# Optimization experiments

Measured on AMD Instinct MI355X. Metric: run time of the kernel, lower is better.

Reference implementation:

```python
import jax, jax.numpy as jnp
import numpy as np

D = 1024
H = 16
DEPTH = D // H


def setup_inputs() -> dict:
    key = jax.random.key(0)
    ks = jax.random.split(key, 10)
    B, S = 4, 2048
    scale = 1.0 / np.sqrt(D)
    x = jax.random.normal(ks[0], (B, S, D), dtype=jnp.float32)
    attention_mask = jnp.ones((B, S, S), dtype=jnp.int32)
    Wq = jax.random.normal(ks[1], (D, D), dtype=jnp.float32) * scale
    bq = jnp.zeros((D,), dtype=jnp.float32)
    Wk = jax.random.normal(ks[2], (D, D), dtype=jnp.float32) * scale
    bk = jnp.zeros((D,), dtype=jnp.float32)
    Wv = jax.random.normal(ks[3], (D, D), dtype=jnp.float32) * scale
    bv = jnp.zeros((D,), dtype=jnp.float32)
    Wo = jax.random.normal(ks[4], (D, D), dtype=jnp.float32) * scale
    bo = jnp.zeros((D,), dtype=jnp.float32)
    return {"x": x, "attention_mask": attention_mask,
            "Wq": Wq, "bq": bq, "Wk": Wk, "bk": bk,
            "Wv": Wv, "bv": bv, "Wo": Wo, "bo": bo}


def _split_heads(t):
    # [b, s, h*d] -> [b, h, s, d]
    b, s, _ = t.shape
    return t.reshape(b, s, H, DEPTH).transpose(0, 2, 1, 3)


def reference(x, attention_mask, Wq, bq, Wk, bk, Wv, bv, Wo, bo):
    # QKV projections (torch Linear: x @ W.T + b; here W stored as [in, out])
    q = _split_heads(x @ Wq + bq)  # [b, h, s, d]
    k = _split_heads(x @ Wk + bk)
    v = _split_heads(x @ Wv + bv)
    scores = jnp.einsum('bhsd,bhtd->bhst', q, k) / jnp.sqrt(jnp.float32(DEPTH))
    mask = attention_mask[:, None, :, :]  # [b, 1, s, s]
    scores = jnp.where(mask == 0, jnp.float32(-jnp.inf), scores)
    attn = jax.nn.softmax(scores, axis=-1)
    # Dropout is identity in eval mode
    out = jnp.einsum('bhst,bhtd->bhsd', attn, v)  # [b, h, s, d]
    b, h, s, d = out.shape
    out = out.transpose(0, 2, 1, 3).reshape(b, s, h * d)
    return out @ Wo + bo
```

## Files before the change

kernel.cpp:

```cpp
#include <hip/hip_runtime.h>
#include <hip/hip_bf16.h>

typedef __bf16 bf16;
typedef __bf16 bf16x4 __attribute__((ext_vector_type(4)));
typedef __bf16 bf16x8 __attribute__((ext_vector_type(8)));
typedef float f32x4 __attribute__((ext_vector_type(4)));

#define AS1 __attribute__((address_space(1)))
#define AS3 __attribute__((address_space(3)))

__device__ __forceinline__ void gload_lds16(const void* g, void* l) {
  __builtin_amdgcn_global_load_lds((const AS1 void*)g, (AS3 void*)l, 16, 0, 0);
}

__device__ __forceinline__ float fexp2(float x) {
#if __has_builtin(__builtin_amdgcn_exp2f)
  return __builtin_amdgcn_exp2f(x);
#else
  return exp2f(x);
#endif
}

#define BB 4
#define SS 2048
#define DD 1024
#define HH 16
#define MM (BB*SS)
#define LDQ 3072
#define NT (SS/64)
#define QSCALE 0.18033688011112042f

__global__ __launch_bounds__(256) void cvt_x(const float* __restrict__ x,
                                             bf16* __restrict__ xb) {
  int i = (blockIdx.x * 256 + threadIdx.x) * 8;
  float4 a = *(const float4*)&x[i];
  float4 b = *(const float4*)&x[i + 4];
  bf16x8 o;
  o[0] = (bf16)a.x; o[1] = (bf16)a.y; o[2] = (bf16)a.z; o[3] = (bf16)a.w;
  o[4] = (bf16)b.x; o[5] = (bf16)b.y; o[6] = (bf16)b.z; o[7] = (bf16)b.w;
  *(bf16x8*)&xb[i] = o;
}

__global__ __launch_bounds__(256) void wtrans4(const float* __restrict__ W0,
                                               const float* __restrict__ W1,
                                               const float* __restrict__ W2,
                                               const float* __restrict__ W3,
                                               bf16* __restrict__ WtQKV,
                                               bf16* __restrict__ Wto) {
  __shared__ float t[64][65];
  const int which = blockIdx.z;
  const float* W = which == 0 ? W0 : which == 1 ? W1 : which == 2 ? W2 : W3;
  bf16* Wt = which < 3 ? WtQKV + (size_t)which * 1024 * DD : Wto;
  const float scale = (which == 0) ? QSCALE : 1.0f;
  int bi = blockIdx.y, bj = blockIdx.x;
  for (int c = 0; c < 16; c++) {
    int idx = threadIdx.x + c * 256;
    int r = idx >> 6, col = idx & 63;
    t[r][col] = W[(size_t)(bi * 64 + r) * DD + bj * 64 + col];
  }
  __syncthreads();
  for (int c = 0; c < 16; c++) {
    int idx = threadIdx.x + c * 256;
    int rn = idx >> 6, ck = idx & 63;
    Wt[(size_t)(bj * 64 + rn) * DD + bi * 64 + ck] = (bf16)(t[ck][rn] * scale);
  }
}

__global__ void bias_cat(const float* __restrict__ bq, const float* __restrict__ bk,
                         const float* __restrict__ bv, float* __restrict__ ball,
                         int* __restrict__ flag) {
  int i = blockIdx.x * 256 + threadIdx.x;
  if (i == 0) *flag = 1;
  float v = (i < 1024) ? bq[i] * QSCALE
                       : ((i < 2048) ? bk[i - 1024] : bv[i - 2048]);
  ball[i] = v;
}

__global__ __launch_bounds__(256) void mask_check(const int4* __restrict__ m,
                                                  int n4, int* flag) {
  int ok = 1;
  for (int i = blockIdx.x * 256 + threadIdx.x; i < n4; i += gridDim.x * 256) {
    int4 v = m[i];
    if (!(v.x && v.y && v.z && v.w)) ok = 0;
  }
  if (__ballot(!ok)) {
    if ((threadIdx.x & 63) == 0) atomicAnd(flag, 0);
  }
}

__global__ __launch_bounds__(256) void vtrans(const bf16* __restrict__ QKV,
                                              bf16* __restrict__ Vt) {
  __shared__ bf16 t[64][80];
  int b = blockIdx.x >> 5, st = blockIdx.x & 31, nt = blockIdx.y;
  int tid = threadIdx.x;
  #pragma unroll
  for (int c = 0; c < 2; c++) {
    int idx = tid + c * 256;
    int r = idx >> 3;
    int c8 = (idx & 7) * 8;
    *(bf16x8*)&t[r][c8] =
        *(const bf16x8*)&QKV[(size_t)(b * SS + st * 64 + r) * LDQ + 2048 +
                             nt * 64 + c8];
  }
  __syncthreads();
  #pragma unroll
  for (int c = 0; c < 2; c++) {
    int idx = tid + c * 256;
    int rn = idx >> 3;
    int s8 = (idx & 7) * 8;
    bf16x8 v;
    #pragma unroll
    for (int j = 0; j < 8; j++) v[j] = t[s8 + j][rn];
    *(bf16x8*)&Vt[(size_t)(b * 1024 + nt * 64 + rn) * SS + st * 64 + s8] = v;
  }
}

template <int OUT_BF16>
__global__ __launch_bounds__(256) void gemm_bt(const bf16* __restrict__ A,
                                               const bf16* __restrict__ Bt,
                                               const float* __restrict__ bias,
                                               void* __restrict__ Cout, int ldc) {
  constexpr int K = 1024;
  constexpr int BM = 128, BN = 128, BK = 64;
  __shared__ bf16 As[BM * BK];
  __shared__ bf16 Bs[BN * BK];
  const int tid = threadIdx.x;
  const int w = tid >> 6, l = tid & 63;
  const int wm = w >> 1, wn = w & 1;
  const int by = blockIdx.x, bx = blockIdx.y;

  f32x4 acc[4][4] = {};

  const int sRow = l >> 3;
  const int sSlot = (l & 7) ^ sRow;
  const bf16* aBase = A + (size_t)(by * BM + w * 32 + sRow) * K + sSlot * 8;
  const bf16* bBase = Bt + (size_t)(bx * BN + w * 32 + sRow) * K + sSlot * 8;

  for (int k0 = 0; k0 < K; k0 += BK) {
    #pragma unroll
    for (int c = 0; c < 4; c++) {
      gload_lds16(aBase + (size_t)(c * 8) * K + k0, &As[(w * 32 + c * 8) * BK]);
      gload_lds16(bBase + (size_t)(c * 8) * K + k0, &Bs[(w * 32 + c * 8) * BK]);
    }
    __syncthreads();
    #pragma unroll
    for (int kk = 0; kk < 2; kk++) {
      bf16x8 af[4], bfr[4];
      #pragma unroll
      for (int i = 0; i < 4; i++) {
        int row = wm * 64 + i * 16 + (l & 15);
        int sl = (kk * 4 + (l >> 4)) ^ (row & 7);
        af[i] = *(const bf16x8*)(&As[row * BK + sl * 8]);
      }
      #pragma unroll
      for (int j = 0; j < 4; j++) {
        int row = wn * 64 + j * 16 + (l & 15);
        int sl = (kk * 4 + (l >> 4)) ^ (row & 7);
        bfr[j] = *(const bf16x8*)(&Bs[row * BK + sl * 8]);
      }
      #pragma unroll
      for (int i = 0; i < 4; i++)
        #pragma unroll
        for (int j = 0; j < 4; j++)
          acc[i][j] = __builtin_amdgcn_mfma_f32_16x16x32_bf16(af[i], bfr[j],
                                                              acc[i][j], 0, 0, 0);
    }
    __syncthreads();
  }

  #pragma unroll
  for (int j = 0; j < 4; j++) {
    int col = bx * BN + wn * 64 + j * 16 + (l & 15);
    float bb = bias[col];
    #pragma unroll
    for (int i = 0; i < 4; i++) {
      int row0 = by * BM + wm * 64 + i * 16 + (l >> 4) * 4;
      #pragma unroll
      for (int r = 0; r < 4; r++) {
        float v = acc[i][j][r] + bb;
        if (OUT_BF16)
          ((bf16*)Cout)[(size_t)(row0 + r) * ldc + col] = (bf16)v;
        else
          ((float*)Cout)[(size_t)(row0 + r) * ldc + col] = v;
      }
    }
  }
}

__global__ __launch_bounds__(256, 2) void attn_fwd(const bf16* __restrict__ QKV,
                                                   const bf16* __restrict__ Vt,
                                                   const int* __restrict__ mask,
                                                   const int* __restrict__ flag,
                                                   bf16* __restrict__ att) {
  __shared__ bf16 Ks[2][64 * 64];
  __shared__ bf16 Vs[2][64 * 64];
  const int tid = threadIdx.x, w = tid >> 6, l = tid & 63;
  const int g = l >> 4, q = l & 15;
  const int bh = blockIdx.x, b = bh >> 4, h = bh & 15;
  const int q0 = blockIdx.y * 256 + w * 64;
  const bool allones = (*flag != 0);

  bf16x8 bq[4][2];
  #pragma unroll
  for (int qb = 0; qb < 4; qb++) {
    const bf16* qptr =
        QKV + (size_t)(b * SS + q0 + qb * 16 + q) * LDQ + h * 64 + g * 8;
    bq[qb][0] = *(const bf16x8*)qptr;
    bq[qb][1] = *(const bf16x8*)(qptr + 32);
  }

  bf16x8 ones;
  #pragma unroll
  for (int j = 0; j < 8; j++) ones[j] = (bf16)1.0f;

  f32x4 o[4][4] = {};
  f32x4 ls[4] = {};

  const int sSlot = (l & 7) ^ ((l >> 3) & 7);
  const bf16* kPtr[2];
  #pragma unroll
  for (int c = 0; c < 2; c++) {
    int B8 = 2 * w + c;
    int tl = 32 * (B8 >> 2) + 16 * (B8 & 1) + 4 * ((B8 >> 1) & 1) +
             8 * (l >> 5) + ((l >> 3) & 3);
    kPtr[c] = QKV + (size_t)(b * SS + tl) * LDQ + 1024 + h * 64 + sSlot * 8;
  }
  const bf16* vBase =
      Vt + (size_t)(b * 1024 + h * 64 + w * 16 + (l >> 3)) * SS + sSlot * 8;

  gload_lds16(kPtr[0], &Ks[0][(2 * w + 0) * 8 * 64]);
  gload_lds16(kPtr[1], &Ks[0][(2 * w + 1) * 8 * 64]);
  gload_lds16(vBase, &Vs[0][(w * 16) * 64]);
  gload_lds16(vBase + (size_t)8 * SS, &Vs[0][(w * 16 + 8) * 64]);

  for (int it = 0; it < NT; ++it) {
    const int cur = it & 1;
    if (it + 1 < NT) {
      const int t1 = (it + 1) * 64;
      gload_lds16(kPtr[0] + (size_t)t1 * LDQ, &Ks[cur ^ 1][(2 * w + 0) * 8 * 64]);
      gload_lds16(kPtr[1] + (size_t)t1 * LDQ, &Ks[cur ^ 1][(2 * w + 1) * 8 * 64]);
      gload_lds16(vBase + t1, &Vs[cur ^ 1][(w * 16) * 64]);
      gload_lds16(vBase + (size_t)8 * SS + t1, &Vs[cur ^ 1][(w * 16 + 8) * 64]);
      asm volatile("s_waitcnt vmcnt(4)" ::: "memory");
    } else {
      asm volatile("s_waitcnt vmcnt(0)" ::: "memory");
    }
    __builtin_amdgcn_s_barrier();
    asm volatile("" ::: "memory");

    const bf16* ks = Ks[cur];
    const bf16* vs = Vs[cur];

    bf16x8 af[4][2];
    #pragma unroll
    for (int tt = 0; tt < 4; tt++) {
      int row = tt * 16 + q;
      af[tt][0] = *(const bf16x8*)(&ks[row * 64 + (g ^ (q & 7)) * 8]);
      af[tt][1] = *(const bf16x8*)(&ks[row * 64 + (((4 + g) ^ (q & 7))) * 8]);
    }

    bf16x8 pb[4][2];
    #pragma unroll
    for (int qb = 0; qb < 4; qb++) {
      f32x4 s4[4];
      #pragma unroll
      for (int tt = 0; tt < 4; tt++) {
        f32x4 z = {};
        z = __builtin_amdgcn_mfma_f32_16x16x32_bf16(af[tt][0], bq[qb][0], z, 0, 0, 0);
        z = __builtin_amdgcn_mfma_f32_16x16x32_bf16(af[tt][1], bq[qb][1], z, 0, 0, 0);
        s4[tt] = z;
      }

      if (!allones) {
        const int t0 = it * 64;
        #pragma unroll
        for (int tt = 0; tt < 4; tt++)
          #pragma unroll
          for (int r = 0; r < 4; r++) {
            int tl = 32 * (tt >> 1) + 8 * g + 4 * (tt & 1) + r;
            if (mask[(size_t)(b * SS + q0 + qb * 16 + q) * SS + t0 + tl] == 0)
              s4[tt][r] = -1e30f;
          }
      }

      #pragma unroll
      for (int kk = 0; kk < 2; kk++) {
        bf16x8 f;
        #pragma unroll
        for (int j = 0; j < 8; j++)
          f[j] = (bf16)fexp2(s4[2 * kk + (j >> 2)][j & 3]);
        pb[qb][kk] = f;
      }
      ls[qb] = __builtin_amdgcn_mfma_f32_16x16x32_bf16(ones, pb[qb][0], ls[qb], 0, 0, 0);
      ls[qb] = __builtin_amdgcn_mfma_f32_16x16x32_bf16(ones, pb[qb][1], ls[qb], 0, 0, 0);
    }

    __builtin_amdgcn_s_setprio(1);
    #pragma unroll
    for (int kk = 0; kk < 2; kk++) {
      int cc = kk * 4 + g;
      #pragma unroll
      for (int n = 0; n < 4; n++) {
        int vrow = n * 16 + q;
        int vsl = cc ^ (q & 7);
        bf16x8 av = *(const bf16x8*)(&vs[vrow * 64 + vsl * 8]);
        #pragma unroll
        for (int qb = 0; qb < 4; qb++)
          o[qb][n] = __builtin_amdgcn_mfma_f32_16x16x32_bf16(av, pb[qb][kk],
                                                             o[qb][n], 0, 0, 0);
      }
    }
    __builtin_amdgcn_s_setprio(0);

    asm volatile("" ::: "memory");
    __builtin_amdgcn_s_barrier();
    asm volatile("" ::: "memory");
  }

  #pragma unroll
  for (int qb = 0; qb < 4; qb++) {
    float inv = 1.0f / ls[qb][0];
    #pragma unroll
    for (int n = 0; n < 4; n++) {
      bf16x4 ov;
      #pragma unroll
      for (int r = 0; r < 4; r++) ov[r] = (bf16)(o[qb][n][r] * inv);
      *(bf16x4*)&att[(size_t)(b * SS + q0 + qb * 16 + q) * DD + h * 64 +
                     n * 16 + g * 4] = ov;
    }
  }
}

extern "C" void kernel_launch(void* const* d_in, const int* in_sizes, int n_in,
                              void* d_out, int out_size, void* d_ws, size_t ws_size,
                              hipStream_t stream) {
  const float* x = (const float*)d_in[0];
  const int* mask = (const int*)d_in[1];
  const float* Wq = (const float*)d_in[2];
  const float* bq = (const float*)d_in[3];
  const float* Wk = (const float*)d_in[4];
  const float* bk = (const float*)d_in[5];
  const float* Wv = (const float*)d_in[6];
  const float* bv = (const float*)d_in[7];
  const float* Wo = (const float*)d_in[8];
  const float* bo = (const float*)d_in[9];
  float* out = (float*)d_out;

  char* p = (char*)d_ws;
  const size_t MB16 = (size_t)MM * DD * 2;
  bf16* xb = (bf16*)p;   p += MB16;
  bf16* QKV = (bf16*)p;  p += (size_t)MM * LDQ * 2;
  bf16* Vt = (bf16*)p;   p += MB16;
  bf16* Wt_all = (bf16*)p; p += (size_t)3072 * DD * 2;
  bf16* Wot = (bf16*)p;  p += (size_t)DD * DD * 2;
  float* ball = (float*)p; p += 3072 * 4;
  int* flag = (int*)p;
  bf16* att = xb;

  bias_cat<<<12, 256, 0, stream>>>(bq, bk, bv, ball, flag);
  mask_check<<<1024, 256, 0, stream>>>((const int4*)mask, BB * SS * SS / 4, flag);
  cvt_x<<<MM * DD / (256 * 8), 256, 0, stream>>>(x, xb);
  wtrans4<<<dim3(16, 16, 4), 256, 0, stream>>>(Wq, Wk, Wv, Wo, Wt_all, Wot);

  gemm_bt<1><<<dim3(64, 24), 256, 0, stream>>>(xb, Wt_all, ball, QKV, LDQ);
  vtrans<<<dim3(128, 16), 256, 0, stream>>>(QKV, Vt);
  attn_fwd<<<dim3(BB * HH, SS / 256), 256, 0, stream>>>(QKV, Vt, mask, flag, att);
  gemm_bt<0><<<dim3(64, 8), 256, 0, stream>>>(att, Wot, bo, out, DD);
}
```

Before: 188.8 us.

## Fuse prep kernels, write V transposed from QKV GEMM, fold mask check into GEMM

Merges the x conversion, weight transposes and bias concatenation into one launch. The QKV GEMM epilogue now writes the V part straight into the transposed Vt buffer, which removes the separate vtrans kernel. The mask all-ones scan moves into the tail of the QKV GEMM. Together these cut kernel launches and a full V round trip through memory. In exchange the GEMM does extra mask reads after its main loop, and the flag init and mask scan now live in different kernels, which relies on stream ordering.

Result: faster. 179.4 us (-5.0%).

```diff
diff --git a/kernel.cpp b/kernel.cpp
--- a/kernel.cpp
+++ b/kernel.cpp
@@ -30,96 +30,59 @@
 #define NT (SS/64)
 #define QSCALE 0.18033688011112042f
 
-__global__ __launch_bounds__(256) void cvt_x(const float* __restrict__ x,
-                                             bf16* __restrict__ xb) {
-  int i = (blockIdx.x * 256 + threadIdx.x) * 8;
-  float4 a = *(const float4*)&x[i];
-  float4 b = *(const float4*)&x[i + 4];
-  bf16x8 o;
-  o[0] = (bf16)a.x; o[1] = (bf16)a.y; o[2] = (bf16)a.z; o[3] = (bf16)a.w;
-  o[4] = (bf16)b.x; o[5] = (bf16)b.y; o[6] = (bf16)b.z; o[7] = (bf16)b.w;
-  *(bf16x8*)&xb[i] = o;
-}
-
-__global__ __launch_bounds__(256) void wtrans4(const float* __restrict__ W0,
-                                               const float* __restrict__ W1,
-                                               const float* __restrict__ W2,
-                                               const float* __restrict__ W3,
-                                               bf16* __restrict__ WtQKV,
-                                               bf16* __restrict__ Wto) {
+__global__ __launch_bounds__(256) void prep(
+    const float* __restrict__ x, bf16* __restrict__ xb,
+    const float* __restrict__ Wq, const float* __restrict__ Wk,
+    const float* __restrict__ Wv, const float* __restrict__ Wo,
+    bf16* __restrict__ WtQKV, bf16* __restrict__ Wto,
+    const float* __restrict__ bq, const float* __restrict__ bk,
+    const float* __restrict__ bv, float* __restrict__ ball,
+    int* __restrict__ flag) {
   __shared__ float t[64][65];
-  const int which = blockIdx.z;
-  const float* W = which == 0 ? W0 : which == 1 ? W1 : which == 2 ? W2 : W3;
-  bf16* Wt = which < 3 ? WtQKV + (size_t)which * 1024 * DD : Wto;
-  const float scale = (which == 0) ? QSCALE : 1.0f;
-  int bi = blockIdx.y, bj = blockIdx.x;
-  for (int c = 0; c < 16; c++) {
-    int idx = threadIdx.x + c * 256;
-    int r = idx >> 6, col = idx & 63;
-    t[r][col] = W[(size_t)(bi * 64 + r) * DD + bj * 64 + col];
-  }
-  __syncthreads();
-  for (int c = 0; c < 16; c++) {
-    int idx = threadIdx.x + c * 256;
-    int rn = idx >> 6, ck = idx & 63;
-    Wt[(size_t)(bj * 64 + rn) * DD + bi * 64 + ck] = (bf16)(t[ck][rn] * scale);
-  }
-}
-
-__global__ void bias_cat(const float* __restrict__ bq, const float* __restrict__ bk,
-                         const float* __restrict__ bv, float* __restrict__ ball,
-                         int* __restrict__ flag) {
-  int i = blockIdx.x * 256 + threadIdx.x;
-  if (i == 0) *flag = 1;
-  float v = (i < 1024) ? bq[i] * QSCALE
-                       : ((i < 2048) ? bk[i - 1024] : bv[i - 2048]);
-  ball[i] = v;
-}
-
-__global__ __launch_bounds__(256) void mask_check(const int4* __restrict__ m,
-                                                  int n4, int* flag) {
-  int ok = 1;
-  for (int i = blockIdx.x * 256 + threadIdx.x; i < n4; i += gridDim.x * 256) {
-    int4 v = m[i];
-    if (!(v.x && v.y && v.z && v.w)) ok = 0;
-  }
-  if (__ballot(!ok)) {
-    if ((threadIdx.x & 63) == 0) atomicAnd(flag, 0);
-  }
-}
-
-__global__ __launch_bounds__(256) void vtrans(const bf16* __restrict__ QKV,
-                                              bf16* __restrict__ Vt) {
-  __shared__ bf16 t[64][80];
-  int b = blockIdx.x >> 5, st = blockIdx.x & 31, nt = blockIdx.y;
-  int tid = threadIdx.x;
-  #pragma unroll
-  for (int c = 0; c < 2; c++) {
-    int idx = tid + c * 256;
-    int r = idx >> 3;
-    int c8 = (idx & 7) * 8;
-    *(bf16x8*)&t[r][c8] =
-        *(const bf16x8*)&QKV[(size_t)(b * SS + st * 64 + r) * LDQ + 2048 +
-                             nt * 64 + c8];
-  }
-  __syncthreads();
-  #pragma unroll
-  for (int c = 0; c < 2; c++) {
-    int idx = tid + c * 256;
-    int rn = idx >> 3;
-    int s8 = (idx & 7) * 8;
-    bf16x8 v;
-    #pragma unroll
-    for (int j = 0; j < 8; j++) v[j] = t[s8 + j][rn];
-    *(bf16x8*)&Vt[(size_t)(b * 1024 + nt * 64 + rn) * SS + st * 64 + s8] = v;
-  }
-}
-
-template <int OUT_BF16>
+  const int bid = blockIdx.x;
+  if (bid < 4096) {
+    int i = (bid * 256 + threadIdx.x) * 8;
+    float4 a = *(const float4*)&x[i];
+    float4 b = *(const float4*)&x[i + 4];
+    bf16x8 o;
+    o[0] = (bf16)a.x; o[1] = (bf16)a.y; o[2] = (bf16)a.z; o[3] = (bf16)a.w;
+    o[4] = (bf16)b.x; o[5] = (bf16)b.y; o[6] = (bf16)b.z; o[7] = (bf16)b.w;
+    *(bf16x8*)&xb[i] = o;
+  } else if (bid < 5120) {
+    int id = bid - 4096;
+    int which = id >> 8;
+    int bi = (id >> 4) & 15, bj = id & 15;
+    const float* W = which == 0 ? Wq : which == 1 ? Wk : which == 2 ? Wv : Wo;
+    bf16* Wt = which < 3 ? WtQKV + (size_t)which * 1024 * DD : Wto;
+    const float scale = (which == 0) ? QSCALE : 1.0f;
+    for (int c = 0; c < 16; c++) {
+      int idx = threadIdx.x + c * 256;
+      int r = idx >> 6, col = idx & 63;
+      t[r][col] = W[(size_t)(bi * 64 + r) * DD + bj * 64 + col];
+    }
+    __syncthreads();
+    for (int c = 0; c < 16; c++) {
+      int idx = threadIdx.x + c * 256;
+      int rn = idx >> 6, ck = idx & 63;
+      Wt[(size_t)(bj * 64 + rn) * DD + bi * 64 + ck] = (bf16)(t[ck][rn] * scale);
+    }
+  } else {
+    int i = (bid - 5120) * 256 + threadIdx.x;
+    if (i == 0) *flag = 1;
+    float v = (i < 1024) ? bq[i] * QSCALE
+                         : ((i < 2048) ? bk[i - 1024] : bv[i - 2048]);
+    ball[i] = v;
+  }
+}
+
+template <int MODE>
 __global__ __launch_bounds__(256) void gemm_bt(const bf16* __restrict__ A,
                                                const bf16* __restrict__ Bt,
                                                const float* __restrict__ bias,
-                                               void* __restrict__ Cout, int ldc) {
+                                               void* __restrict__ Cout, int ldc,
+                                               bf16* __restrict__ Vt,
+                                               const int4* __restrict__ mask4,
+                                               int* __restrict__ flag) {
   constexpr int K = 1024;
   constexpr int BM = 128, BN = 128, BK = 64;
   __shared__ bf16 As[BM * BK];
@@ -168,21 +131,53 @@
     __syncthreads();
   }
 
-  #pragma unroll
-  for (int j = 0; j < 4; j++) {
-    int col = bx * BN + wn * 64 + j * 16 + (l & 15);
-    float bb = bias[col];
-    #pragma unroll
-    for (int i = 0; i < 4; i++) {
-      int row0 = by * BM + wm * 64 + i * 16 + (l >> 4) * 4;
-      #pragma unroll
-      for (int r = 0; r < 4; r++) {
-        float v = acc[i][j][r] + bb;
-        if (OUT_BF16)
-          ((bf16*)Cout)[(size_t)(row0 + r) * ldc + col] = (bf16)v;
-        else
-          ((float*)Cout)[(size_t)(row0 + r) * ldc + col] = v;
-      }
+  if (MODE == 2 && bx >= 16) {
+    #pragma unroll
+    for (int j = 0; j < 4; j++) {
+      int col = bx * BN + wn * 64 + j * 16 + (l & 15);
+      int n = col - 2048;
+      float bb = bias[col];
+      #pragma unroll
+      for (int i = 0; i < 4; i++) {
+        int row0 = by * BM + wm * 64 + i * 16 + (l >> 4) * 4;
+        int b_ = row0 >> 11;
+        int s0 = row0 & 2047;
+        bf16x4 vv;
+        #pragma unroll
+        for (int r = 0; r < 4; r++) vv[r] = (bf16)(acc[i][j][r] + bb);
+        *(bf16x4*)&Vt[(size_t)(b_ * 1024 + n) * SS + s0] = vv;
+      }
+    }
+  } else {
+    #pragma unroll
+    for (int j = 0; j < 4; j++) {
+      int col = bx * BN + wn * 64 + j * 16 + (l & 15);
+      float bb = bias[col];
+      #pragma unroll
+      for (int i = 0; i < 4; i++) {
+        int row0 = by * BM + wm * 64 + i * 16 + (l >> 4) * 4;
+        #pragma unroll
+        for (int r = 0; r < 4; r++) {
+          float v = acc[i][j][r] + bb;
+          if (MODE == 2)
+            ((bf16*)Cout)[(size_t)(row0 + r) * ldc + col] = (bf16)v;
+          else
+            ((float*)Cout)[(size_t)(row0 + r) * ldc + col] = v;
+        }
+      }
+    }
+  }
+
+  if (MODE == 2) {
+    const int n4 = BB * SS * SS / 4;
+    const int lin = by * 24 + bx;
+    int ok = 1;
+    for (int i = lin * 256 + tid; i < n4; i += 1536 * 256) {
+      int4 v = mask4[i];
+      if (!(v.x && v.y && v.z && v.w)) ok = 0;
+    }
+    if (__ballot(!ok)) {
+      if ((tid & 63) == 0) atomicAnd(flag, 0);
     }
   }
 }
@@ -357,13 +352,11 @@
   int* flag = (int*)p;
   bf16* att = xb;
 
-  bias_cat<<<12, 256, 0, stream>>>(bq, bk, bv, ball, flag);
-  mask_check<<<1024, 256, 0, stream>>>((const int4*)mask, BB * SS * SS / 4, flag);
-  cvt_x<<<MM * DD / (256 * 8), 256, 0, stream>>>(x, xb);
-  wtrans4<<<dim3(16, 16, 4), 256, 0, stream>>>(Wq, Wk, Wv, Wo, Wt_all, Wot);
-
-  gemm_bt<1><<<dim3(64, 24), 256, 0, stream>>>(xb, Wt_all, ball, QKV, LDQ);
-  vtrans<<<dim3(128, 16), 256, 0, stream>>>(QKV, Vt);
+  prep<<<5132, 256, 0, stream>>>(x, xb, Wq, Wk, Wv, Wo, Wt_all, Wot,
+                                 bq, bk, bv, ball, flag);
+  gemm_bt<2><<<dim3(64, 24), 256, 0, stream>>>(xb, Wt_all, ball, QKV, LDQ,
+                                               Vt, (const int4*)mask, flag);
   attn_fwd<<<dim3(BB * HH, SS / 256), 256, 0, stream>>>(QKV, Vt, mask, flag, att);
-  gemm_bt<0><<<dim3(64, 8), 256, 0, stream>>>(att, Wot, bo, out, DD);
-}
+  gemm_bt<0><<<dim3(64, 8), 256, 0, stream>>>(att, Wot, bo, out, DD,
+                                              Vt, (const int4*)mask, flag);
+}
```
